# Optimization experiments

Hardware: AMD Instinct MI355X
Metric: run time of the kernel (lower is better)

## Reference

```python
import jax, jax.numpy as jnp
import numpy as np

B, S, C, D, H, FF, DEPTH, T, N = 8, 1024, 2, 512, 8, 2048, 6, 64, 16
HD = D // H
EPS = 1e-5


def _ln(x, w, b):
    m = jnp.mean(x, axis=-1, keepdims=True)
    v = jnp.mean(jnp.square(x - m), axis=-1, keepdims=True)
    return (x - m) * jax.lax.rsqrt(v + EPS) * w + b


def setup_inputs() -> dict:
    key = jax.random.key(0)
    ks = jax.random.split(key, 24)
    w = lambda k, shape: (jax.random.normal(k, shape, jnp.float32) * 0.02)
    return {
        "src": jax.random.normal(ks[0], (B, S, D), jnp.float32),
        "ctx_emb": jax.random.normal(ks[1], (B, C, D), jnp.float32),
        "times": jax.random.randint(ks[2], (B, S), 0, T),
        "spaces": jax.random.randint(ks[3], (B, S), 0, N),
        "pad_mask": jnp.zeros((B, S + C), bool),
        "time_emb": w(ks[4], (T, D)),
        "space_emb": w(ks[5], (N, D)),
        "Wqkv": w(ks[6], (DEPTH, 3 * D, D)),
        "bqkv": jnp.zeros((DEPTH, 3 * D), jnp.float32),
        "Wo": w(ks[7], (DEPTH, D, D)),
        "bo": jnp.zeros((DEPTH, D), jnp.float32),
        "ln1_w": jnp.ones((DEPTH, D), jnp.float32),
        "ln1_b": jnp.zeros((DEPTH, D), jnp.float32),
        "W1": w(ks[8], (DEPTH, FF, D)),
        "b1": jnp.zeros((DEPTH, FF), jnp.float32),
        "W2": w(ks[9], (DEPTH, D, FF)),
        "b2": jnp.zeros((DEPTH, D), jnp.float32),
        "ln2_w": jnp.ones((DEPTH, D), jnp.float32),
        "ln2_b": jnp.zeros((DEPTH, D), jnp.float32),
    }


def _forward(src, ctx_emb, times, spaces, pad_mask, time_emb, space_emb,
             Wqkv, bqkv, Wo, bo, ln1_w, ln1_b, W1, b1, W2, b2, ln2_w, ln2_b):
    NEG = -jnp.inf
    # learned time/space positional embeddings, then append context tokens
    x = src + time_emb[times] + space_emb[spaces]          # [B,S,D]
    x = jnp.concatenate([x, ctx_emb], axis=1)              # [B,L,D], L=S+C
    # per-batch additive float mask: causal-in-time over src tokens,
    # ctx tokens attendable by everyone, ctx rows attend only to ctx.
    cond = times[:, :, None] >= times[:, None, :]          # [B,S,S]
    m = jnp.where(cond, 0.0, NEG)
    m = jnp.pad(m, ((0, 0), (0, C), (0, 0)), constant_values=NEG)  # ctx rows
    m = jnp.pad(m, ((0, 0), (0, 0), (0, C)), constant_values=0.0)  # ctx cols
    m = m + jnp.where(pad_mask[:, None, :], NEG, 0.0)      # key padding
    m = m[:, None]                                         # [B,1,L,L]

    scale = 1.0 / np.sqrt(HD)
    Bc, L, _ = x.shape
    for i in range(DEPTH):
        # --- self-attention (post-norm encoder layer) ---
        qkv = x @ Wqkv[i].T + bqkv[i]                      # [B,L,3D]
        q, k, v = jnp.split(qkv, 3, axis=-1)
        split = lambda t: t.reshape(Bc, L, H, HD).transpose(0, 2, 1, 3)
        q, k, v = split(q), split(k), split(v)             # [B,H,L,HD]
        scores = jnp.einsum('bhqd,bhkd->bhqk', q, k) * scale + m
        p = jax.nn.softmax(scores, axis=-1)
        a = jnp.einsum('bhqk,bhkd->bhqd', p, v)
        a = a.transpose(0, 2, 1, 3).reshape(Bc, L, D)
        a = a @ Wo[i].T + bo[i]
        x = _ln(x + a, ln1_w[i], ln1_b[i])
        # --- feed-forward ---
        h = jax.nn.gelu(x @ W1[i].T + b1[i], approximate=False)
        h = h @ W2[i].T + b2[i]
        x = _ln(x + h, ln2_w[i], ln2_b[i])
    return x[:, :S]                                        # drop ctx tokens


def reference(src, ctx_emb, times, spaces, pad_mask, time_emb, space_emb,
              Wqkv, bqkv, Wo, bo, ln1_w, ln1_b, W1, b1, W2, b2, ln2_w, ln2_b):
    return _forward(src, ctx_emb, times, spaces, pad_mask, time_emb, space_emb,
                    Wqkv, bqkv, Wo, bo, ln1_w, ln1_b, W1, b1, W2, b2, ln2_w, ln2_b)
```

## Files before the change

### kernel.cpp

```cpp
#include <hip/hip_runtime.h>
#include <hip/hip_bf16.h>

#define BB 8
#define SS 1024
#define CC 2
#define DD 512
#define NH 8
#define FF2 2048
#define NL 6
#define LL 1026
#define HD 64
#define MROWS 8208
#define MP 8320
#define KVPAD 1152

typedef __attribute__((ext_vector_type(8))) short bf16x8;
typedef __attribute__((ext_vector_type(4))) float f32x4;

typedef __attribute__((address_space(3))) void lds_void;
typedef __attribute__((address_space(1))) void g_void;

__device__ __forceinline__ void gll16(const void* g, void* l) {
  __builtin_amdgcn_global_load_lds((const g_void*)g, (lds_void*)l, 16, 0, 0);
}

__global__ __launch_bounds__(256) void cvt_bf16_k(const float* __restrict__ in,
                                                  __hip_bfloat16* __restrict__ out) {
  int i = (blockIdx.x * 256 + threadIdx.x) * 4;
  float4 v = *(const float4*)&in[i];
  out[i + 0] = __float2bfloat16(v.x);
  out[i + 1] = __float2bfloat16(v.y);
  out[i + 2] = __float2bfloat16(v.z);
  out[i + 3] = __float2bfloat16(v.w);
}

__global__ __launch_bounds__(256) void embed_k(const float* __restrict__ src,
    const float* __restrict__ ctx, const int* __restrict__ times,
    const int* __restrict__ spaces, const float* __restrict__ te,
    const float* __restrict__ se, float* __restrict__ x,
    __hip_bfloat16* __restrict__ xb) {
  int row = blockIdx.x;
  int b = row / LL, l = row % LL;
  int c = threadIdx.x * 2;
  float y0, y1;
  if (l < SS) {
    const float* sp = src + ((size_t)(b * SS + l)) * DD + c;
    int tt = times[b * SS + l], ssp = spaces[b * SS + l];
    y0 = sp[0] + te[tt * DD + c] + se[ssp * DD + c];
    y1 = sp[1] + te[tt * DD + c + 1] + se[ssp * DD + c + 1];
  } else {
    const float* cp = ctx + ((size_t)(b * CC + (l - SS))) * DD + c;
    y0 = cp[0]; y1 = cp[1];
  }
  size_t o = (size_t)row * DD + c;
  x[o] = y0; x[o + 1] = y1;
  xb[o] = __float2bfloat16(y0); xb[o + 1] = __float2bfloat16(y1);
}

template <int EPI>
__global__ __launch_bounds__(256) void gemm_bt(const __hip_bfloat16* __restrict__ A,
    const __hip_bfloat16* __restrict__ W, const float* __restrict__ bias,
    void* __restrict__ outp, int K, int N) {
  __shared__ __hip_bfloat16 As[64 * 64];
  __shared__ __hip_bfloat16 Bs[128 * 64];
  const int tid = threadIdx.x;
  const int lane = tid & 63, wv = tid >> 6;
  const int ny = N >> 7;
  const int nwg = gridDim.x;
  int qq = nwg >> 3, rr = nwg & 7;
  int xcd = blockIdx.x & 7, loc = blockIdx.x >> 3;
  int slot = (xcd < rr ? xcd * (qq + 1) : rr * (qq + 1) + (xcd - rr) * qq) + loc;
  const int m0 = (slot / ny) * 64, n0 = (slot % ny) * 128;
  const int r0 = lane & 15, kq = lane >> 4;
  f32x4 acc[4][2] = {};
  for (int k0 = 0; k0 < K; k0 += 64) {
    __syncthreads();
#pragma unroll
    for (int c = 0; c < 6; ++c) {
      int ch = c * 256 + tid;
      if (ch < 512) {
        int row = ch >> 3, cp = ch & 7;
        gll16(A + (size_t)(m0 + row) * K + k0 + cp * 8, (char*)As + ch * 16);
      } else {
        int bi = ch - 512;
        int row = bi >> 3, cp = bi & 7;
        gll16(W + (size_t)(n0 + row) * K + k0 + cp * 8, (char*)Bs + bi * 16);
      }
    }
    __syncthreads();
#pragma unroll
    for (int kk = 0; kk < 64; kk += 32) {
      bf16x8 af[4], bfr[2];
#pragma unroll
      for (int m = 0; m < 4; ++m)
        af[m] = *(const bf16x8*)&As[(m * 16 + r0) * 64 + kk + kq * 8];
#pragma unroll
      for (int n = 0; n < 2; ++n)
        bfr[n] = *(const bf16x8*)&Bs[(wv * 32 + n * 16 + r0) * 64 + kk + kq * 8];
#pragma unroll
      for (int m = 0; m < 4; ++m)
#pragma unroll
        for (int n = 0; n < 2; ++n)
          acc[m][n] = __builtin_amdgcn_mfma_f32_16x16x32_bf16(af[m], bfr[n], acc[m][n], 0, 0, 0);
    }
  }
#pragma unroll
  for (int m = 0; m < 4; ++m) {
    int grow_base = m0 + m * 16 + kq * 4;
#pragma unroll
    for (int n = 0; n < 2; ++n) {
      int gcol = n0 + wv * 32 + n * 16 + r0;
      float bv = (EPI == 0) ? 0.f : bias[gcol];
#pragma unroll
      for (int j = 0; j < 4; ++j) {
        int grow = grow_base + j;
        float v = acc[m][n][j] + bv;
        ((__hip_bfloat16*)outp)[(size_t)grow * N + gcol] = __float2bfloat16(v);
      }
    }
  }
}

template <int EPI>
__global__ __launch_bounds__(512) void gemm_bt2(const __hip_bfloat16* __restrict__ A,
    const __hip_bfloat16* __restrict__ W, const float* __restrict__ bias,
    void* __restrict__ outp, int K, int N) {
  __shared__ __hip_bfloat16 As[128 * 64];
  __shared__ __hip_bfloat16 Bs[256 * 64];
  const int tid = threadIdx.x;
  const int lane = tid & 63, wv = tid >> 6;
  const int ny = N >> 8;
  const int nwg = gridDim.x;
  int qq = nwg >> 3, rr = nwg & 7;
  int xcd = blockIdx.x & 7, loc = blockIdx.x >> 3;
  int slot = (xcd < rr ? xcd * (qq + 1) : rr * (qq + 1) + (xcd - rr) * qq) + loc;
  const int m0 = (slot / ny) * 128, n0 = (slot % ny) * 256;
  const int wr = wv >> 2, wc = wv & 3;
  const int r0 = lane & 15, kq = lane >> 4;
  f32x4 acc[4][4] = {};
  for (int k0 = 0; k0 < K; k0 += 64) {
    __syncthreads();
#pragma unroll
    for (int c = 0; c < 6; ++c) {
      int ch = c * 512 + tid;
      if (ch < 1024) {
        int row = ch >> 3, cp = ch & 7;
        gll16(A + (size_t)(m0 + row) * K + k0 + cp * 8, (char*)As + ch * 16);
      } else {
        int bi = ch - 1024;
        int row = bi >> 3, cp = bi & 7;
        gll16(W + (size_t)(n0 + row) * K + k0 + cp * 8, (char*)Bs + bi * 16);
      }
    }
    __syncthreads();
#pragma unroll
    for (int kk = 0; kk < 64; kk += 32) {
      bf16x8 af[4], bfr[4];
#pragma unroll
      for (int m = 0; m < 4; ++m)
        af[m] = *(const bf16x8*)&As[(wr * 64 + m * 16 + r0) * 64 + kk + kq * 8];
#pragma unroll
      for (int n = 0; n < 4; ++n)
        bfr[n] = *(const bf16x8*)&Bs[(wc * 64 + n * 16 + r0) * 64 + kk + kq * 8];
#pragma unroll
      for (int m = 0; m < 4; ++m)
#pragma unroll
        for (int n = 0; n < 4; ++n)
          acc[m][n] = __builtin_amdgcn_mfma_f32_16x16x32_bf16(af[m], bfr[n], acc[m][n], 0, 0, 0);
    }
  }
#pragma unroll
  for (int m = 0; m < 4; ++m) {
    int grow_base = m0 + wr * 64 + m * 16 + kq * 4;
#pragma unroll
    for (int n = 0; n < 4; ++n) {
      int gcol = n0 + wc * 64 + n * 16 + r0;
      float bv = (EPI == 0) ? 0.f : bias[gcol];
#pragma unroll
      for (int j = 0; j < 4; ++j) {
        int grow = grow_base + j;
        float v = acc[m][n][j] + bv;
        if (EPI == 2) v = 0.5f * v * (1.f + erff(v * 0.70710678f));
        ((__hip_bfloat16*)outp)[(size_t)grow * N + gcol] = __float2bfloat16(v);
      }
    }
  }
}

__global__ __launch_bounds__(256) void vtrans_k(const __hip_bfloat16* __restrict__ qkv,
                                                __hip_bfloat16* __restrict__ vt) {
  __shared__ __hip_bfloat16 tile[64][72];
  int bh = blockIdx.y;
  int b = bh >> 3, hh = bh & 7;
  int l0 = blockIdx.x * 64;
  int t = threadIdx.x;
  int lr = t >> 2, part = t & 3;
  int l = l0 + lr;
  if (l < LL) {
    const __hip_bfloat16* p = qkv + (size_t)(b * LL + l) * 1536 + 1024 + hh * 64 + part * 16;
    *(uint4*)&tile[lr][part * 16] = *(const uint4*)p;
    *(uint4*)&tile[lr][part * 16 + 8] = *(const uint4*)(p + 8);
  } else {
    uint4 z = make_uint4(0, 0, 0, 0);
    *(uint4*)&tile[lr][part * 16] = z;
    *(uint4*)&tile[lr][part * 16 + 8] = z;
  }
  __syncthreads();
  int d = t >> 2, kp = t & 3;
  __hip_bfloat16 vals[16];
#pragma unroll
  for (int i = 0; i < 16; ++i) vals[i] = tile[kp * 16 + i][d];
  __hip_bfloat16* o = vt + ((size_t)(bh * 64 + d)) * KVPAD + l0 + kp * 16;
  *(uint4*)o = *(uint4*)&vals[0];
  *(uint4*)(o + 8) = *(uint4*)&vals[8];
}

#define TK_CTX (-2000000000)
#define TQ_CTX (-1000000000)
#define TK_INV (2000000000)

__global__ __launch_bounds__(256) void attn_k(const __hip_bfloat16* __restrict__ qkv,
    const __hip_bfloat16* __restrict__ vt, const int* __restrict__ times,
    __hip_bfloat16* __restrict__ aout) {
  __shared__ __hip_bfloat16 Kl[128 * 64];
  __shared__ __hip_bfloat16 Vl[64 * 128];
  __shared__ __hip_bfloat16 Pl[4][16 * 128];
  const int tid = threadIdx.x, lane = tid & 63, wv = tid >> 6;
  const int r0 = lane & 15, kq = lane >> 4;
  int i = blockIdx.x;
  int xcd = i & 7, slot = i >> 3;
  int bhl = slot / 17;
  int qb = slot - bhl * 17;
  int bh = xcd * 8 + bhl;
  int b = bh >> 3, hh = bh & 7;
  char* plbase = (char*)&Pl[wv][0];

  const int qbase = qb * 64 + wv * 16;
  int qr = qbase + r0;
  if (qr > LL - 1) qr = LL - 1;
  const __hip_bfloat16* qp = qkv + (size_t)(b * LL + qr) * 1536 + hh * 64;
  bf16x8 qa0 = *(const bf16x8*)(qp + kq * 8);
  bf16x8 qa1 = *(const bf16x8*)(qp + 32 + kq * 8);
  int tq[4];
#pragma unroll
  for (int j = 0; j < 4; ++j) {
    int r = qbase + kq * 4 + j;
    tq[j] = (r < SS) ? times[b * SS + r] : TQ_CTX;
  }
  float m_run[4] = {-1e30f, -1e30f, -1e30f, -1e30f};
  float l_run[4] = {0.f, 0.f, 0.f, 0.f};
  f32x4 O[4] = {};
  const float scale = 0.125f;

  for (int kc = 0; kc < 9; ++kc) {
    __syncthreads();
#pragma unroll
    for (int c = 0; c < 4; ++c) {
      int chb = c * 256 + wv * 64;
      int ch = chb + lane;
      {
        int trow = ch >> 3, cp = ch & 7;
        int krow = kc * 128 + trow;
        if (krow > LL - 1) krow = LL - 1;
        int scp = cp ^ (trow & 7);
        gll16(qkv + (size_t)(b * LL + krow) * 1536 + 512 + hh * 64 + scp * 8,
              (char*)Kl + chb * 16);
      }
      {
        int d = ch >> 4, kp = ch & 15;
        int skp = kp ^ (d & 7);
        gll16(vt + ((size_t)(bh * 64 + d)) * KVPAD + kc * 128 + skp * 8,
              (char*)Vl + chb * 16);
      }
    }
    __syncthreads();
    f32x4 s[8] = {};
#pragma unroll
    for (int n = 0; n < 8; ++n) {
      int row = n * 16 + r0;
      bf16x8 kb0 = *(const bf16x8*)&Kl[row * 64 + ((kq ^ (row & 7)) * 8)];
      bf16x8 kb1 = *(const bf16x8*)&Kl[row * 64 + (((4 + kq) ^ (row & 7)) * 8)];
      s[n] = __builtin_amdgcn_mfma_f32_16x16x32_bf16(qa0, kb0, s[n], 0, 0, 0);
      s[n] = __builtin_amdgcn_mfma_f32_16x16x32_bf16(qa1, kb1, s[n], 0, 0, 0);
    }
    int tkn[8];
#pragma unroll
    for (int n = 0; n < 8; ++n) {
      int k = kc * 128 + 16 * n + r0;
      tkn[n] = (k < SS) ? times[b * SS + k] : ((k < LL) ? TK_CTX : TK_INV);
    }
    float mch[4] = {-1e30f, -1e30f, -1e30f, -1e30f};
#pragma unroll
    for (int n = 0; n < 8; ++n)
#pragma unroll
      for (int j = 0; j < 4; ++j) {
        float sv = (tq[j] >= tkn[n]) ? s[n][j] * scale : -1e30f;
        s[n][j] = sv;
        mch[j] = fmaxf(mch[j], sv);
      }
#pragma unroll
    for (int j = 0; j < 4; ++j) {
#pragma unroll
      for (int off = 1; off < 16; off <<= 1)
        mch[j] = fmaxf(mch[j], __shfl_xor(mch[j], off, 64));
    }
    float fac[4], psum[4];
#pragma unroll
    for (int j = 0; j < 4; ++j) {
      float mn = fmaxf(m_run[j], mch[j]);
      fac[j] = __expf(m_run[j] - mn);
      m_run[j] = mn;
      psum[j] = 0.f;
    }
#pragma unroll
    for (int n = 0; n < 8; ++n)
#pragma unroll
      for (int j = 0; j < 4; ++j) {
        float p = __expf(s[n][j] - m_run[j]);
        s[n][j] = p;
        psum[j] += p;
      }
#pragma unroll
    for (int j = 0; j < 4; ++j) {
#pragma unroll
      for (int off = 1; off < 16; off <<= 1)
        psum[j] += __shfl_xor(psum[j], off, 64);
      l_run[j] = l_run[j] * fac[j] + psum[j];
    }
#pragma unroll
    for (int n = 0; n < 4; ++n)
#pragma unroll
      for (int j = 0; j < 4; ++j) O[n][j] *= fac[j];
#pragma unroll
    for (int n = 0; n < 8; ++n)
#pragma unroll
      for (int j = 0; j < 4; ++j) {
        int q = kq * 4 + j;
        int byte = ((r0 + 16 * n) * 2) ^ ((q & 7) << 4);
        *(__hip_bfloat16*)(plbase + q * 256 + byte) = __float2bfloat16(s[n][j]);
      }
#pragma unroll
    for (int c = 0; c < 4; ++c) {
      int rbyte = (c * 64 + kq * 16) ^ ((r0 & 7) << 4);
      bf16x8 pa = *(const bf16x8*)(plbase + r0 * 256 + rbyte);
#pragma unroll
      for (int n = 0; n < 4; ++n) {
        int d = n * 16 + r0;
        int chv = (c * 4 + kq) ^ (r0 & 7);
        bf16x8 vb = *(const bf16x8*)&Vl[d * 128 + chv * 8];
        O[n] = __builtin_amdgcn_mfma_f32_16x16x32_bf16(pa, vb, O[n], 0, 0, 0);
      }
    }
  }
#pragma unroll
  for (int j = 0; j < 4; ++j) {
    int orow = qbase + kq * 4 + j;
    if (orow < LL) {
      float inv = 1.f / l_run[j];
#pragma unroll
      for (int n = 0; n < 4; ++n)
        aout[(size_t)(b * LL + orow) * DD + hh * 64 + n * 16 + r0] =
            __float2bfloat16(O[n][j] * inv);
    }
  }
}

__global__ __launch_bounds__(256) void ln_fuse_k(float* __restrict__ x,
    const __hip_bfloat16* __restrict__ tmp, const float* __restrict__ gb,
    const float* __restrict__ w, const float* __restrict__ bias,
    __hip_bfloat16* __restrict__ xb) {
  const int row = blockIdx.x;
  const int tid = threadIdx.x;
  size_t o = (size_t)row * DD + tid * 2;
  float2 v = *(const float2*)&x[o];
  const __hip_bfloat16* tp = tmp + o;
  float t0 = __bfloat162float(tp[0]);
  float t1 = __bfloat162float(tp[1]);
  float a0 = v.x + gb[tid * 2] + t0, a1 = v.y + gb[tid * 2 + 1] + t1;
  float s = a0 + a1, ss = a0 * a0 + a1 * a1;
#pragma unroll
  for (int off = 1; off < 64; off <<= 1) {
    s += __shfl_xor(s, off, 64);
    ss += __shfl_xor(ss, off, 64);
  }
  __shared__ float red[8];
  const int wv = tid >> 6, lane = tid & 63;
  if (lane == 0) { red[wv] = s; red[4 + wv] = ss; }
  __syncthreads();
  s = red[0] + red[1] + red[2] + red[3];
  ss = red[4] + red[5] + red[6] + red[7];
  float mean = s * (1.f / 512.f);
  float var = ss * (1.f / 512.f) - mean * mean;
  if (var < 0.f) var = 0.f;
  float rs = rsqrtf(var + 1e-5f);
  float w0 = w[tid * 2], w1 = w[tid * 2 + 1];
  float b0 = bias[tid * 2], b1 = bias[tid * 2 + 1];
  float y0 = (a0 - mean) * rs * w0 + b0;
  float y1 = (a1 - mean) * rs * w1 + b1;
  x[o] = y0; x[o + 1] = y1;
  xb[o] = __float2bfloat16(y0); xb[o + 1] = __float2bfloat16(y1);
}

__global__ __launch_bounds__(256) void copy_out_k(const float* __restrict__ x,
                                                  float* __restrict__ out) {
  size_t i = ((size_t)blockIdx.x * 256 + threadIdx.x) * 4;
  int b = (int)(i >> 19);
  int rem = (int)(i & 524287);
  float4 v = *(const float4*)&x[(size_t)b * LL * DD + rem];
  *(float4*)&out[i] = v;
}

extern "C" void kernel_launch(void* const* d_in, const int* in_sizes, int n_in,
                              void* d_out, int out_size, void* d_ws, size_t ws_size,
                              hipStream_t stream) {
  (void)in_sizes; (void)n_in; (void)out_size; (void)ws_size;
  const float* src    = (const float*)d_in[0];
  const float* ctx    = (const float*)d_in[1];
  const int*   times  = (const int*)d_in[2];
  const int*   spaces = (const int*)d_in[3];
  const float* te     = (const float*)d_in[5];
  const float* se     = (const float*)d_in[6];
  const float* Wqkv   = (const float*)d_in[7];
  const float* bqkv   = (const float*)d_in[8];
  const float* Wo     = (const float*)d_in[9];
  const float* bo     = (const float*)d_in[10];
  const float* ln1w   = (const float*)d_in[11];
  const float* ln1b   = (const float*)d_in[12];
  const float* W1     = (const float*)d_in[13];
  const float* b1     = (const float*)d_in[14];
  const float* W2     = (const float*)d_in[15];
  const float* b2     = (const float*)d_in[16];
  const float* ln2w   = (const float*)d_in[17];
  const float* ln2b   = (const float*)d_in[18];

  char* ws = (char*)d_ws;
  size_t off = 0;
  auto alloc = [&](size_t bytes) {
    size_t o = off;
    off += (bytes + 255) & ~(size_t)255;
    return o;
  };
  float* x            = (float*)(ws + alloc((size_t)MP * DD * 4));
  __hip_bfloat16* xb  = (__hip_bfloat16*)(ws + alloc((size_t)MP * DD * 2));
  __hip_bfloat16* qkv = (__hip_bfloat16*)(ws + alloc((size_t)MP * 3 * DD * 2));
  __hip_bfloat16* abf = (__hip_bfloat16*)(ws + alloc((size_t)MP * DD * 2));
  __hip_bfloat16* hbf = (__hip_bfloat16*)(ws + alloc((size_t)MP * FF2 * 2));
  __hip_bfloat16* tmp = (__hip_bfloat16*)(ws + alloc((size_t)MP * DD * 2));
  __hip_bfloat16* vt  = (__hip_bfloat16*)(ws + alloc((size_t)BB * NH * HD * KVPAD * 2));
  __hip_bfloat16* wqb = (__hip_bfloat16*)(ws + alloc((size_t)NL * 3 * DD * DD * 2));
  __hip_bfloat16* wob = (__hip_bfloat16*)(ws + alloc((size_t)NL * DD * DD * 2));
  __hip_bfloat16* w1b = (__hip_bfloat16*)(ws + alloc((size_t)NL * FF2 * DD * 2));
  __hip_bfloat16* w2b = (__hip_bfloat16*)(ws + alloc((size_t)NL * DD * FF2 * 2));

  cvt_bf16_k<<<(NL * 3 * DD * DD) / 1024, 256, 0, stream>>>(Wqkv, wqb);
  cvt_bf16_k<<<(NL * DD * DD) / 1024, 256, 0, stream>>>(Wo, wob);
  cvt_bf16_k<<<(NL * FF2 * DD) / 1024, 256, 0, stream>>>(W1, w1b);
  cvt_bf16_k<<<(NL * DD * FF2) / 1024, 256, 0, stream>>>(W2, w2b);

  embed_k<<<MROWS, 256, 0, stream>>>(src, ctx, times, spaces, te, se, x, xb);

  for (int i = 0; i < NL; ++i) {
    gemm_bt2<1><<<65 * 6, 512, 0, stream>>>(
        xb, wqb + (size_t)i * 3 * DD * DD, bqkv + i * 3 * DD, qkv, DD, 3 * DD);
    vtrans_k<<<dim3(17, BB * NH), 256, 0, stream>>>(qkv, vt);
    attn_k<<<1088, 256, 0, stream>>>(qkv, vt, times, abf);
    gemm_bt<0><<<130 * 4, 256, 0, stream>>>(
        abf, wob + (size_t)i * DD * DD, nullptr, tmp, DD, DD);
    ln_fuse_k<<<MROWS, 256, 0, stream>>>(x, tmp, bo + i * DD,
                                         ln1w + i * DD, ln1b + i * DD, xb);
    gemm_bt2<2><<<65 * 8, 512, 0, stream>>>(
        xb, w1b + (size_t)i * FF2 * DD, b1 + i * FF2, hbf, DD, FF2);
    gemm_bt<0><<<130 * 4, 256, 0, stream>>>(
        hbf, w2b + (size_t)i * DD * FF2, nullptr, tmp, FF2, DD);
    ln_fuse_k<<<MROWS, 256, 0, stream>>>(x, tmp, b2 + i * DD,
                                         ln2w + i * DD, ln2b + i * DD, xb);
  }

  copy_out_k<<<(BB * SS * DD) / 1024, 256, 0, stream>>>(x, (float*)d_out);
}
```

Measured before the change: 1.424 ms.

## Fuse V transpose into QKV GEMM epilogue and final copy into layernorm

The QKV GEMM epilogue now writes Q and K into a narrower 1024-wide buffer and scatters V directly into the transposed per-head layout, so the separate vtrans kernel is no longer needed. The last layer's second layernorm writes the output rows directly, which removes the copy_out kernel. The vt buffer is zeroed once up front so its padded tail stays valid. The V scatter writes single bf16 values with a large stride, which coalesces poorly and may slow the GEMM epilogue.

```diff
diff --git a/kernel.cpp b/kernel.cpp
--- a/kernel.cpp
+++ b/kernel.cpp
@@ -22,6 +22,10 @@
 
 __device__ __forceinline__ void gll16(const void* g, void* l) {
   __builtin_amdgcn_global_load_lds((const g_void*)g, (lds_void*)l, 16, 0, 0);
+}
+
+__global__ __launch_bounds__(256) void zero_k(float4* __restrict__ p) {
+  p[(size_t)blockIdx.x * 256 + threadIdx.x] = make_float4(0.f, 0.f, 0.f, 0.f);
 }
 
 __global__ __launch_bounds__(256) void cvt_bf16_k(const float* __restrict__ in,
@@ -124,7 +128,7 @@
 template <int EPI>
 __global__ __launch_bounds__(512) void gemm_bt2(const __hip_bfloat16* __restrict__ A,
     const __hip_bfloat16* __restrict__ W, const float* __restrict__ bias,
-    void* __restrict__ outp, int K, int N) {
+    void* __restrict__ outp, __hip_bfloat16* __restrict__ vtp, int K, int N) {
   __shared__ __hip_bfloat16 As[128 * 64];
   __shared__ __hip_bfloat16 Bs[256 * 64];
   const int tid = threadIdx.x;
@@ -175,51 +179,36 @@
 #pragma unroll
     for (int n = 0; n < 4; ++n) {
       int gcol = n0 + wc * 64 + n * 16 + r0;
-      float bv = (EPI == 0) ? 0.f : bias[gcol];
+      float bv = bias[gcol];
 #pragma unroll
       for (int j = 0; j < 4; ++j) {
         int grow = grow_base + j;
         float v = acc[m][n][j] + bv;
-        if (EPI == 2) v = 0.5f * v * (1.f + erff(v * 0.70710678f));
-        ((__hip_bfloat16*)outp)[(size_t)grow * N + gcol] = __float2bfloat16(v);
-      }
-    }
-  }
-}
-
-__global__ __launch_bounds__(256) void vtrans_k(const __hip_bfloat16* __restrict__ qkv,
-                                                __hip_bfloat16* __restrict__ vt) {
-  __shared__ __hip_bfloat16 tile[64][72];
-  int bh = blockIdx.y;
-  int b = bh >> 3, hh = bh & 7;
-  int l0 = blockIdx.x * 64;
-  int t = threadIdx.x;
-  int lr = t >> 2, part = t & 3;
-  int l = l0 + lr;
-  if (l < LL) {
-    const __hip_bfloat16* p = qkv + (size_t)(b * LL + l) * 1536 + 1024 + hh * 64 + part * 16;
-    *(uint4*)&tile[lr][part * 16] = *(const uint4*)p;
-    *(uint4*)&tile[lr][part * 16 + 8] = *(const uint4*)(p + 8);
-  } else {
-    uint4 z = make_uint4(0, 0, 0, 0);
-    *(uint4*)&tile[lr][part * 16] = z;
-    *(uint4*)&tile[lr][part * 16 + 8] = z;
-  }
-  __syncthreads();
-  int d = t >> 2, kp = t & 3;
-  __hip_bfloat16 vals[16];
-#pragma unroll
-  for (int i = 0; i < 16; ++i) vals[i] = tile[kp * 16 + i][d];
-  __hip_bfloat16* o = vt + ((size_t)(bh * 64 + d)) * KVPAD + l0 + kp * 16;
-  *(uint4*)o = *(uint4*)&vals[0];
-  *(uint4*)(o + 8) = *(uint4*)&vals[8];
+        if (EPI == 2) {
+          v = 0.5f * v * (1.f + erff(v * 0.70710678f));
+          ((__hip_bfloat16*)outp)[(size_t)grow * N + gcol] = __float2bfloat16(v);
+        } else {
+          if (grow < MROWS) {
+            if (gcol < 1024) {
+              ((__hip_bfloat16*)outp)[(size_t)grow * 1024 + gcol] = __float2bfloat16(v);
+            } else {
+              int b = grow / LL, l = grow - b * LL;
+              int hd = gcol - 1024;
+              int hh = hd >> 6, d = hd & 63;
+              vtp[((size_t)((b * NH + hh) * 64 + d)) * KVPAD + l] = __float2bfloat16(v);
+            }
+          }
+        }
+      }
+    }
+  }
 }
 
 #define TK_CTX (-2000000000)
 #define TQ_CTX (-1000000000)
 #define TK_INV (2000000000)
 
-__global__ __launch_bounds__(256) void attn_k(const __hip_bfloat16* __restrict__ qkv,
+__global__ __launch_bounds__(256) void attn_k(const __hip_bfloat16* __restrict__ qk,
     const __hip_bfloat16* __restrict__ vt, const int* __restrict__ times,
     __hip_bfloat16* __restrict__ aout) {
   __shared__ __hip_bfloat16 Kl[128 * 64];
@@ -238,7 +227,7 @@
   const int qbase = qb * 64 + wv * 16;
   int qr = qbase + r0;
   if (qr > LL - 1) qr = LL - 1;
-  const __hip_bfloat16* qp = qkv + (size_t)(b * LL + qr) * 1536 + hh * 64;
+  const __hip_bfloat16* qp = qk + (size_t)(b * LL + qr) * 1024 + hh * 64;
   bf16x8 qa0 = *(const bf16x8*)(qp + kq * 8);
   bf16x8 qa1 = *(const bf16x8*)(qp + 32 + kq * 8);
   int tq[4];
@@ -263,7 +252,7 @@
         int krow = kc * 128 + trow;
         if (krow > LL - 1) krow = LL - 1;
         int scp = cp ^ (trow & 7);
-        gll16(qkv + (size_t)(b * LL + krow) * 1536 + 512 + hh * 64 + scp * 8,
+        gll16(qk + (size_t)(b * LL + krow) * 1024 + 512 + hh * 64 + scp * 8,
               (char*)Kl + chb * 16);
       }
       {
@@ -368,7 +357,7 @@
 __global__ __launch_bounds__(256) void ln_fuse_k(float* __restrict__ x,
     const __hip_bfloat16* __restrict__ tmp, const float* __restrict__ gb,
     const float* __restrict__ w, const float* __restrict__ bias,
-    __hip_bfloat16* __restrict__ xb) {
+    __hip_bfloat16* __restrict__ xb, float* __restrict__ fout) {
   const int row = blockIdx.x;
   const int tid = threadIdx.x;
   size_t o = (size_t)row * DD + tid * 2;
@@ -399,15 +388,13 @@
   float y1 = (a1 - mean) * rs * w1 + b1;
   x[o] = y0; x[o + 1] = y1;
   xb[o] = __float2bfloat16(y0); xb[o + 1] = __float2bfloat16(y1);
-}
-
-__global__ __launch_bounds__(256) void copy_out_k(const float* __restrict__ x,
-                                                  float* __restrict__ out) {
-  size_t i = ((size_t)blockIdx.x * 256 + threadIdx.x) * 4;
-  int b = (int)(i >> 19);
-  int rem = (int)(i & 524287);
-  float4 v = *(const float4*)&x[(size_t)b * LL * DD + rem];
-  *(float4*)&out[i] = v;
+  if (fout != nullptr) {
+    int b = row / LL, l = row - b * LL;
+    if (l < SS) {
+      float* fp = fout + ((size_t)(b * SS + l)) * DD + tid * 2;
+      fp[0] = y0; fp[1] = y1;
+    }
+  }
 }
 
 extern "C" void kernel_launch(void* const* d_in, const int* in_sizes, int n_in,
@@ -442,7 +429,7 @@
   };
   float* x            = (float*)(ws + alloc((size_t)MP * DD * 4));
   __hip_bfloat16* xb  = (__hip_bfloat16*)(ws + alloc((size_t)MP * DD * 2));
-  __hip_bfloat16* qkv = (__hip_bfloat16*)(ws + alloc((size_t)MP * 3 * DD * 2));
+  __hip_bfloat16* qk  = (__hip_bfloat16*)(ws + alloc((size_t)MP * 1024 * 2));
   __hip_bfloat16* abf = (__hip_bfloat16*)(ws + alloc((size_t)MP * DD * 2));
   __hip_bfloat16* hbf = (__hip_bfloat16*)(ws + alloc((size_t)MP * FF2 * 2));
   __hip_bfloat16* tmp = (__hip_bfloat16*)(ws + alloc((size_t)MP * DD * 2));
@@ -452,6 +439,9 @@
   __hip_bfloat16* w1b = (__hip_bfloat16*)(ws + alloc((size_t)NL * FF2 * DD * 2));
   __hip_bfloat16* w2b = (__hip_bfloat16*)(ws + alloc((size_t)NL * DD * FF2 * 2));
 
+  const int vtN = (int)(((size_t)BB * NH * HD * KVPAD * 2) / (256 * 16));
+  zero_k<<<vtN, 256, 0, stream>>>((float4*)vt);
+
   cvt_bf16_k<<<(NL * 3 * DD * DD) / 1024, 256, 0, stream>>>(Wqkv, wqb);
   cvt_bf16_k<<<(NL * DD * DD) / 1024, 256, 0, stream>>>(Wo, wob);
   cvt_bf16_k<<<(NL * FF2 * DD) / 1024, 256, 0, stream>>>(W1, w1b);
@@ -460,21 +450,19 @@
   embed_k<<<MROWS, 256, 0, stream>>>(src, ctx, times, spaces, te, se, x, xb);
 
   for (int i = 0; i < NL; ++i) {
-    gemm_bt2<1><<<65 * 6, 512, 0, stream>>>(
-        xb, wqb + (size_t)i * 3 * DD * DD, bqkv + i * 3 * DD, qkv, DD, 3 * DD);
-    vtrans_k<<<dim3(17, BB * NH), 256, 0, stream>>>(qkv, vt);
-    attn_k<<<1088, 256, 0, stream>>>(qkv, vt, times, abf);
+    gemm_bt2<3><<<65 * 6, 512, 0, stream>>>(
+        xb, wqb + (size_t)i * 3 * DD * DD, bqkv + i * 3 * DD, qk, vt, DD, 3 * DD);
+    attn_k<<<1088, 256, 0, stream>>>(qk, vt, times, abf);
     gemm_bt<0><<<130 * 4, 256, 0, stream>>>(
         abf, wob + (size_t)i * DD * DD, nullptr, tmp, DD, DD);
     ln_fuse_k<<<MROWS, 256, 0, stream>>>(x, tmp, bo + i * DD,
-                                         ln1w + i * DD, ln1b + i * DD, xb);
+                                         ln1w + i * DD, ln1b + i * DD, xb, nullptr);
     gemm_bt2<2><<<65 * 8, 512, 0, stream>>>(
-        xb, w1b + (size_t)i * FF2 * DD, b1 + i * FF2, hbf, DD, FF2);
+        xb, w1b + (size_t)i * FF2 * DD, b1 + i * FF2, hbf, nullptr, DD, FF2);
     gemm_bt<0><<<130 * 4, 256, 0, stream>>>(
         hbf, w2b + (size_t)i * DD * FF2, nullptr, tmp, FF2, DD);
     ln_fuse_k<<<MROWS, 256, 0, stream>>>(x, tmp, b2 + i * DD,
-                                         ln2w + i * DD, ln2b + i * DD, xb);
-  }
-
-  copy_out_k<<<(BB * SS * DD) / 1024, 256, 0, stream>>>(x, (float*)d_out);
-}
+                                         ln2w + i * DD, ln2b + i * DD, xb,
+                                         (i == NL - 1) ? (float*)d_out : nullptr);
+  }
+}
```

Result: slower. 1.474 ms (+3.5%).
